# Kernel optimization log

Hardware: AMD Instinct MI355X
Metric: run time of the kernel (lower is better)

The kernel has to match this reference:

```python
import jax, jax.numpy as jnp
import numpy as np

B, S, D, V, ND = 8, 512, 1024, 32000, 8


def setup_inputs() -> dict:
    key = jax.random.key(0)
    k1, k2, k3, k4 = jax.random.split(key, 4)
    scale = 0.02
    return {
        "hidden_states": jax.random.normal(k1, (B, S, D), dtype=jnp.float32),
        "domain_ids": jax.random.randint(k2, (B,), 0, ND + 1),  # index ND triggers default head
        "W_base": jax.random.normal(k3, (D, D), dtype=jnp.float32) * scale,
        "b_base": jnp.zeros((D,), dtype=jnp.float32),
        # slots 0..ND-1 are domain heads, slot ND is the default head
        "W_heads": jax.random.normal(k4, (ND + 1, D, V), dtype=jnp.float32) * scale,
        "b_heads": jnp.zeros((ND + 1, V), dtype=jnp.float32),
    }


def reference(hidden_states, domain_ids, W_base, b_base, W_heads, b_heads):
    # base_projection: Linear(D, D)
    hidden = jnp.einsum("bsd,de->bse", hidden_states, W_base) + b_base
    num_domains = W_heads.shape[0] - 1
    # out-of-range domain ids fall back to the default head (last slot)
    idx = jnp.where((domain_ids >= 0) & (domain_ids < num_domains), domain_ids, num_domains)
    Wg = W_heads[idx]              # [B, D, V] gathered per-example head weights
    bg = b_heads[idx]              # [B, V]
    out = jnp.einsum("bsd,bdv->bsv", hidden, Wg) + bg[:, None, :]
    return out
```

## Files before the change

kernel.cpp:

```cpp
#include <hip/hip_runtime.h>
#include <hip/hip_bf16.h>


#define BCNT 8
#define SLEN 512
#define DDIM 1024
#define VDIM 32000
#define NDOM 8

typedef __attribute__((ext_vector_type(4))) float f32x4;
typedef __attribute__((ext_vector_type(8))) short bf16x8;

static __device__ __forceinline__ unsigned short f2bf(float f) {
    union { float f; unsigned int u; } x; x.f = f;
    unsigned int u = x.u;
    return (unsigned short)((u + 0x7FFFu + ((u >> 16) & 1u)) >> 16);
}

static __device__ __forceinline__ unsigned int pack2(float lo, float hi) {
    float2 t; t.x = lo; t.y = hi;
    union { __hip_bfloat162 h; unsigned int u; } c;
    c.h = __float22bfloat162_rn(t);
    return c.u;
}

#define SBAR()   __builtin_amdgcn_s_barrier()
#define SCHED0() __builtin_amdgcn_sched_barrier(0)

__global__ __launch_bounds__(256)
void gemm1_k(const float* __restrict__ Af, const float* __restrict__ Bbase,
             const float* __restrict__ bias, __hip_bfloat16* __restrict__ Cb,
             int Mrows)
{
    __shared__ __align__(16) __hip_bfloat16 lds_a[128 * 64];
    __shared__ __align__(16) unsigned int   lds_b[32 * 128];

    const int tid  = threadIdx.x;
    const int lane = tid & 63;
    const int w    = tid >> 6;

    const int nwg = gridDim.x;
    const int bid = blockIdx.x;
    const int q   = nwg >> 3;
    const int sid = (bid & 7) * q + (bid >> 3);

    const int MT = Mrows >> 7;
    const int mt = sid % MT;
    const int nt = sid / MT;
    const int m0 = mt << 7;
    const int n0 = nt << 7;

    f32x4 acc[4][4];
    #pragma unroll
    for (int m = 0; m < 4; ++m)
        #pragma unroll
        for (int n = 0; n < 4; ++n)
            acc[m][n] = (f32x4)0.0f;

    const int wr = w >> 1, wc = w & 1;
    const int lr = lane & 15, lg = lane >> 4;

    for (int kt = 0; kt < DDIM / 64; ++kt) {
        const int kbase = kt * 64;

        #pragma unroll
        for (int t = 0; t < 8; ++t) {
            const int flat = (t * 256 + tid) * 4;
            const int row = flat >> 6, col = flat & 63;
            const float4 v = *(const float4*)(Af + (size_t)(m0 + row) * DDIM + kbase + col);
            uint2 pp;
            pp.x = pack2(v.x, v.y);
            pp.y = pack2(v.z, v.w);
            *(uint2*)(lds_a + flat) = pp;
        }

        #pragma unroll
        for (int t = 0; t < 4; ++t) {
            const int id = t * 256 + tid;
            const int kk = id >> 5;
            const int n  = (id & 31) << 2;
            const float* b0 = Bbase + (size_t)(kbase + 2 * kk) * DDIM + n0 + n;
            const float4 e = *(const float4*)b0;
            const float4 o = *(const float4*)(b0 + DDIM);
            uint4 pw;
            pw.x = pack2(e.x, o.x);
            pw.y = pack2(e.y, o.y);
            pw.z = pack2(e.z, o.z);
            pw.w = pack2(e.w, o.w);
            const int ns = n ^ ((kk & 4) << 2);
            *(uint4*)&lds_b[kk * 128 + ns] = pw;
        }

        __syncthreads();

        #pragma unroll
        for (int ks = 0; ks < 2; ++ks) {
            bf16x8 af[4], bfr[4];
            #pragma unroll
            for (int m = 0; m < 4; ++m) {
                const int row = wr * 64 + m * 16 + lr;
                const int k   = ks * 32 + lg * 8;
                af[m] = *(const bf16x8*)&lds_a[row * 64 + k];
            }
            #pragma unroll
            for (int n = 0; n < 4; ++n) {
                const int col = wc * 64 + n * 16 + lr;
                const int kkb = ks * 16 + lg * 4;
                union { unsigned int u[4]; bf16x8 v; } cvt;
                #pragma unroll
                for (int j = 0; j < 4; ++j) {
                    const int kk = kkb + j;
                    const int ns = col ^ ((kk & 4) << 2);
                    cvt.u[j] = lds_b[kk * 128 + ns];
                }
                bfr[n] = cvt.v;
            }
            #pragma unroll
            for (int m = 0; m < 4; ++m)
                #pragma unroll
                for (int n = 0; n < 4; ++n)
                    acc[m][n] = __builtin_amdgcn_mfma_f32_16x16x32_bf16(af[m], bfr[n], acc[m][n], 0, 0, 0);
        }

        __syncthreads();
    }

    #pragma unroll
    for (int m = 0; m < 4; ++m) {
        #pragma unroll
        for (int n = 0; n < 4; ++n) {
            const int col = n0 + wc * 64 + n * 16 + lr;
            const float bv = bias[col];
            #pragma unroll
            for (int r = 0; r < 4; ++r) {
                const int row = m0 + wr * 64 + m * 16 + lg * 4 + r;
                Cb[(size_t)row * DDIM + col] = __hip_bfloat16_raw{f2bf(acc[m][n][r] + bv)};
            }
        }
    }
}

__global__ __launch_bounds__(512, 4)
void gemm2_k(const __hip_bfloat16* __restrict__ A, const float* __restrict__ Wh,
             const float* __restrict__ bh, float* __restrict__ out,
             const int* __restrict__ dom)
{
    __shared__ __align__(16) __hip_bfloat16 ldsA[256 * 64];
    __shared__ __align__(16) unsigned int   ldsB[128 * 32];

    const int tid  = threadIdx.x;
    const int lane = tid & 63;
    const int w    = tid >> 6;
    const int wr   = w >> 1;
    const int wc   = w & 1;
    const int lr   = lane & 15;
    const int lg   = lane >> 4;

    const int bid  = blockIdx.x;
    const int q    = gridDim.x >> 3;
    const int sid  = (bid & 7) * q + (bid >> 3);
    const int mt   = sid & 1;
    const int rest = sid >> 1;
    const int nt   = rest % 250;
    const int ex   = rest / 250;
    const int m0   = ex * SLEN + mt * 256;
    const int n0   = nt * 128;

    const int di  = dom[ex];
    const int hid = (di >= 0 && di < NDOM) ? di : NDOM;
    const float* Bp   = Wh + (size_t)hid * DDIM * (size_t)VDIM;
    const float* bias = bh + (size_t)hid * (size_t)VDIM;

    f32x4 acc[4][4];
    #pragma unroll
    for (int m = 0; m < 4; ++m)
        #pragma unroll
        for (int n = 0; n < 4; ++n)
            acc[m][n] = (f32x4)0.0f;

    const int nb  = (tid & 63) << 1;
    const int kb  = (tid >> 6) << 3;
    const int qb  = kb >> 1;
    const int bsw = (lane & 7) << 2;
    const int bslot = qb ^ bsw;

    float2 br[8];

    #define LOADB(KT) do {                                                         \
        const float* _p = Bp + (size_t)((KT) * 64 + kb) * VDIM + n0 + nb;          \
        _Pragma("unroll")                                                          \
        for (int j = 0; j < 8; ++j) br[j] = *(const float2*)(_p + (size_t)j * VDIM); \
    } while (0)

    #define WRITEB() do {                                                          \
        uint4 w0, w1;                                                              \
        w0.x = pack2(br[0].x, br[1].x); w0.y = pack2(br[2].x, br[3].x);            \
        w0.z = pack2(br[4].x, br[5].x); w0.w = pack2(br[6].x, br[7].x);            \
        w1.x = pack2(br[0].y, br[1].y); w1.y = pack2(br[2].y, br[3].y);            \
        w1.z = pack2(br[4].y, br[5].y); w1.w = pack2(br[6].y, br[7].y);            \
        *(uint4*)&ldsB[nb * 32 + bslot]       = w0;                                \
        *(uint4*)&ldsB[(nb + 1) * 32 + bslot] = w1;                                \
    } while (0)

    #define STAGEA(KT) do {                                                        \
        _Pragma("unroll")                                                          \
        for (int i = 0; i < 4; ++i) {                                              \
            const int base_e = (i * 8 + w) * 512;                                  \
            const int flat   = base_e + lane * 8;                                  \
            const int row    = flat >> 6;                                          \
            const int kbyte  = (flat & 63) * 2;                                    \
            const int srck   = (kbyte ^ ((row & 7) << 4)) >> 1;                    \
            const __hip_bfloat16* src = A + (size_t)(m0 + row) * DDIM + (KT) * 64 + srck; \
            __builtin_amdgcn_global_load_lds(                                      \
                (const __attribute__((address_space(1))) unsigned int*)src,        \
                (__attribute__((address_space(3))) unsigned int*)(ldsA + base_e),  \
                16, 0, 0);                                                         \
        }                                                                          \
    } while (0)

    #define COMPUTE() do {                                                         \
        _Pragma("unroll")                                                          \
        for (int ks = 0; ks < 2; ++ks) {                                           \
            bf16x8 af[4], bfr[4];                                                  \
            _Pragma("unroll")                                                      \
            for (int m = 0; m < 4; ++m) {                                          \
                const int row = wr * 64 + m * 16 + lr;                             \
                const int kby = ks * 64 + lg * 16;                                 \
                const int eff = kby ^ ((row & 7) << 4);                            \
                af[m] = *(const bf16x8*)&ldsA[row * 64 + (eff >> 1)];              \
            }                                                                      \
            _Pragma("unroll")                                                      \
            for (int n = 0; n < 4; ++n) {                                          \
                const int col  = wc * 64 + n * 16 + lr;                            \
                const int kkb  = ks * 16 + lg * 4;                                 \
                const int slot = kkb ^ (((col >> 1) & 7) << 2);                    \
                bfr[n] = *(const bf16x8*)&ldsB[col * 32 + slot];                   \
            }                                                                      \
            _Pragma("unroll")                                                      \
            for (int m = 0; m < 4; ++m)                                            \
                _Pragma("unroll")                                                  \
                for (int n = 0; n < 4; ++n)                                        \
                    acc[m][n] = __builtin_amdgcn_mfma_f32_16x16x32_bf16(af[m], bfr[n], acc[m][n], 0, 0, 0); \
        }                                                                          \
    } while (0)

    LOADB(0);
    SCHED0();
    STAGEA(0);
    SCHED0();
    WRITEB();
    SCHED0();
    LOADB(1);
    SCHED0();
    asm volatile("s_waitcnt vmcnt(8) lgkmcnt(0)" ::: "memory");
    SCHED0();
    SBAR();

    for (int kt = 0; kt < 16; ++kt) {
        COMPUTE();
        if (kt < 15) {
            SCHED0();
            SBAR();
            SCHED0();
            STAGEA(kt + 1);
            SCHED0();
            WRITEB();
            SCHED0();
            if (kt < 14) {
                LOADB(kt + 2);
                SCHED0();
                asm volatile("s_waitcnt vmcnt(8) lgkmcnt(0)" ::: "memory");
            } else {
                asm volatile("s_waitcnt vmcnt(0) lgkmcnt(0)" ::: "memory");
            }
            SCHED0();
            SBAR();
        }
    }

    #pragma unroll
    for (int n = 0; n < 4; ++n) {
        const int col = n0 + wc * 64 + n * 16 + lr;
        const float bv = bias[col];
        #pragma unroll
        for (int m = 0; m < 4; ++m) {
            #pragma unroll
            for (int r = 0; r < 4; ++r) {
                const int row = m0 + wr * 64 + m * 16 + lg * 4 + r;
                out[(size_t)row * VDIM + col] = acc[m][n][r] + bv;
            }
        }
    }

    #undef LOADB
    #undef WRITEB
    #undef STAGEA
    #undef COMPUTE
}

extern "C" void kernel_launch(void* const* d_in, const int* in_sizes, int n_in,
                              void* d_out, int out_size, void* d_ws, size_t ws_size,
                              hipStream_t stream)
{
    const float* hs  = (const float*)d_in[0];
    const int*   dom = (const int*)d_in[1];
    const float* Wb  = (const float*)d_in[2];
    const float* bb  = (const float*)d_in[3];
    const float* Wh  = (const float*)d_in[4];
    const float* bh  = (const float*)d_in[5];
    float* out = (float*)d_out;
    __hip_bfloat16* hidden = (__hip_bfloat16*)d_ws;

    const int M = BCNT * SLEN;

    const int g1 = (M / 128) * (DDIM / 128);
    hipLaunchKernelGGL(gemm1_k, dim3(g1), dim3(256), 0, stream, hs, Wb, bb, hidden, M);

    const int g2 = BCNT * (SLEN / 256) * (VDIM / 128);
    hipLaunchKernelGGL(gemm2_k, dim3(g2), dim3(512), 0, stream, hidden, Wh, bh, out, dom);
}
```

Before: 531.4 us.

## Double-buffer LDS in head GEMM and interleave staging with MFMA half-steps

Switches the second GEMM from single-buffered to double-buffered LDS for both the A and B tiles, using 96KB of dynamic shared memory. Each k-step is split into two halves so global-to-LDS staging for the next tile overlaps with MFMA on the current one, and MFMA phases get raised wave priority. This is meant to hide load and barrier latency, at the cost of halving the occupancy target (launch bounds 4→2) and adding more barriers per iteration.

```diff
diff --git a/kernel.cpp b/kernel.cpp
--- a/kernel.cpp
+++ b/kernel.cpp
@@ -140,13 +140,16 @@
     }
 }
 
-__global__ __launch_bounds__(512, 4)
+__global__ __launch_bounds__(512, 2)
 void gemm2_k(const __hip_bfloat16* __restrict__ A, const float* __restrict__ Wh,
              const float* __restrict__ bh, float* __restrict__ out,
              const int* __restrict__ dom)
 {
-    __shared__ __align__(16) __hip_bfloat16 ldsA[256 * 64];
-    __shared__ __align__(16) unsigned int   ldsB[128 * 32];
+    extern __shared__ __align__(16) char smem[];
+    __hip_bfloat16* ldsA0 = (__hip_bfloat16*)smem;
+    __hip_bfloat16* ldsA1 = (__hip_bfloat16*)(smem + 32768);
+    unsigned int*   ldsB0 = (unsigned int*)(smem + 65536);
+    unsigned int*   ldsB1 = (unsigned int*)(smem + 81920);
 
     const int tid  = threadIdx.x;
     const int lane = tid & 63;
@@ -192,19 +195,19 @@
         for (int j = 0; j < 8; ++j) br[j] = *(const float2*)(_p + (size_t)j * VDIM); \
     } while (0)
 
-    #define WRITEB() do {                                                          \
+    #define WRITEB(LB) do {                                                        \
         uint4 w0, w1;                                                              \
         w0.x = pack2(br[0].x, br[1].x); w0.y = pack2(br[2].x, br[3].x);            \
         w0.z = pack2(br[4].x, br[5].x); w0.w = pack2(br[6].x, br[7].x);            \
         w1.x = pack2(br[0].y, br[1].y); w1.y = pack2(br[2].y, br[3].y);            \
         w1.z = pack2(br[4].y, br[5].y); w1.w = pack2(br[6].y, br[7].y);            \
-        *(uint4*)&ldsB[nb * 32 + bslot]       = w0;                                \
-        *(uint4*)&ldsB[(nb + 1) * 32 + bslot] = w1;                                \
-    } while (0)
-
-    #define STAGEA(KT) do {                                                        \
-        _Pragma("unroll")                                                          \
-        for (int i = 0; i < 4; ++i) {                                              \
+        *(uint4*)&(LB)[nb * 32 + bslot]       = w0;                                \
+        *(uint4*)&(LB)[(nb + 1) * 32 + bslot] = w1;                                \
+    } while (0)
+
+    #define STAGEA_H(LA, KT, H) do {                                               \
+        _Pragma("unroll")                                                          \
+        for (int i = 2*(H); i < 2*(H) + 2; ++i) {                                  \
             const int base_e = (i * 8 + w) * 512;                                  \
             const int flat   = base_e + lane * 8;                                  \
             const int row    = flat >> 6;                                          \
@@ -213,42 +216,42 @@
             const __hip_bfloat16* src = A + (size_t)(m0 + row) * DDIM + (KT) * 64 + srck; \
             __builtin_amdgcn_global_load_lds(                                      \
                 (const __attribute__((address_space(1))) unsigned int*)src,        \
-                (__attribute__((address_space(3))) unsigned int*)(ldsA + base_e),  \
+                (__attribute__((address_space(3))) unsigned int*)((LA) + base_e),  \
                 16, 0, 0);                                                         \
         }                                                                          \
     } while (0)
 
-    #define COMPUTE() do {                                                         \
-        _Pragma("unroll")                                                          \
-        for (int ks = 0; ks < 2; ++ks) {                                           \
-            bf16x8 af[4], bfr[4];                                                  \
+    #define READ_FRAGS(AF, BF, LA, LB, KS) do {                                    \
+        _Pragma("unroll")                                                          \
+        for (int m = 0; m < 4; ++m) {                                              \
+            const int row = wr * 64 + m * 16 + lr;                                 \
+            const int kby = (KS) * 64 + lg * 16;                                   \
+            const int eff = kby ^ ((row & 7) << 4);                                \
+            AF[m] = *(const bf16x8*)&(LA)[row * 64 + (eff >> 1)];                  \
+        }                                                                          \
+        _Pragma("unroll")                                                          \
+        for (int n = 0; n < 4; ++n) {                                              \
+            const int col  = wc * 64 + n * 16 + lr;                                \
+            const int kkb  = (KS) * 16 + lg * 4;                                   \
+            const int slot = kkb ^ (((col >> 1) & 7) << 2);                        \
+            BF[n] = *(const bf16x8*)&(LB)[col * 32 + slot];                        \
+        }                                                                          \
+    } while (0)
+
+    #define MFMA16(AF, BF) do {                                                    \
+        _Pragma("unroll")                                                          \
+        for (int m = 0; m < 4; ++m)                                                \
             _Pragma("unroll")                                                      \
-            for (int m = 0; m < 4; ++m) {                                          \
-                const int row = wr * 64 + m * 16 + lr;                             \
-                const int kby = ks * 64 + lg * 16;                                 \
-                const int eff = kby ^ ((row & 7) << 4);                            \
-                af[m] = *(const bf16x8*)&ldsA[row * 64 + (eff >> 1)];              \
-            }                                                                      \
-            _Pragma("unroll")                                                      \
-            for (int n = 0; n < 4; ++n) {                                          \
-                const int col  = wc * 64 + n * 16 + lr;                            \
-                const int kkb  = ks * 16 + lg * 4;                                 \
-                const int slot = kkb ^ (((col >> 1) & 7) << 2);                    \
-                bfr[n] = *(const bf16x8*)&ldsB[col * 32 + slot];                   \
-            }                                                                      \
-            _Pragma("unroll")                                                      \
-            for (int m = 0; m < 4; ++m)                                            \
-                _Pragma("unroll")                                                  \
-                for (int n = 0; n < 4; ++n)                                        \
-                    acc[m][n] = __builtin_amdgcn_mfma_f32_16x16x32_bf16(af[m], bfr[n], acc[m][n], 0, 0, 0); \
-        }                                                                          \
+            for (int n = 0; n < 4; ++n)                                            \
+                acc[m][n] = __builtin_amdgcn_mfma_f32_16x16x32_bf16(AF[m], BF[n], acc[m][n], 0, 0, 0); \
     } while (0)
 
     LOADB(0);
     SCHED0();
-    STAGEA(0);
-    SCHED0();
-    WRITEB();
+    STAGEA_H(ldsA0, 0, 0);
+    STAGEA_H(ldsA0, 0, 1);
+    SCHED0();
+    WRITEB(ldsB0);
     SCHED0();
     LOADB(1);
     SCHED0();
@@ -257,24 +260,51 @@
     SBAR();
 
     for (int kt = 0; kt < 16; ++kt) {
-        COMPUTE();
-        if (kt < 15) {
-            SCHED0();
+        __hip_bfloat16* lA  = (kt & 1) ? ldsA1 : ldsA0;
+        __hip_bfloat16* lAn = (kt & 1) ? ldsA0 : ldsA1;
+        unsigned int*   lB  = (kt & 1) ? ldsB1 : ldsB0;
+        unsigned int*   lBn = (kt & 1) ? ldsB0 : ldsB1;
+
+        {
+            bf16x8 af[4], bfr[4];
+            READ_FRAGS(af, bfr, lA, lB, 0);
+            SCHED0();
+            if (kt < 15) { STAGEA_H(lAn, kt + 1, 0); SCHED0(); }
             SBAR();
-            SCHED0();
-            STAGEA(kt + 1);
-            SCHED0();
-            WRITEB();
+            asm volatile("s_waitcnt lgkmcnt(0)" ::: "memory");
+            SCHED0();
+            __builtin_amdgcn_s_setprio(1);
+            MFMA16(af, bfr);
+            __builtin_amdgcn_s_setprio(0);
+            SCHED0();
+            SBAR();
+        }
+
+        {
+            bf16x8 af[4], bfr[4];
+            READ_FRAGS(af, bfr, lA, lB, 1);
+            SCHED0();
+            if (kt < 15) {
+                STAGEA_H(lAn, kt + 1, 1);
+                SCHED0();
+                WRITEB(lBn);
+                SCHED0();
+            }
+            if (kt < 14) { LOADB(kt + 2); SCHED0(); }
+            SBAR();
+            asm volatile("s_waitcnt lgkmcnt(0)" ::: "memory");
+            SCHED0();
+            __builtin_amdgcn_s_setprio(1);
+            MFMA16(af, bfr);
+            __builtin_amdgcn_s_setprio(0);
             SCHED0();
             if (kt < 14) {
-                LOADB(kt + 2);
-                SCHED0();
-                asm volatile("s_waitcnt vmcnt(8) lgkmcnt(0)" ::: "memory");
-            } else {
-                asm volatile("s_waitcnt vmcnt(0) lgkmcnt(0)" ::: "memory");
-            }
-            SCHED0();
-            SBAR();
+                asm volatile("s_waitcnt vmcnt(8)" ::: "memory");
+            } else if (kt == 14) {
+                asm volatile("s_waitcnt vmcnt(0)" ::: "memory");
+            }
+            SCHED0();
+            if (kt < 15) SBAR();
         }
     }
 
@@ -294,8 +324,9 @@
 
     #undef LOADB
     #undef WRITEB
-    #undef STAGEA
-    #undef COMPUTE
+    #undef STAGEA_H
+    #undef READ_FRAGS
+    #undef MFMA16
 }
 
 extern "C" void kernel_launch(void* const* d_in, const int* in_sizes, int n_in,
@@ -316,6 +347,12 @@
     const int g1 = (M / 128) * (DDIM / 128);
     hipLaunchKernelGGL(gemm1_k, dim3(g1), dim3(256), 0, stream, hs, Wb, bb, hidden, M);
 
+    const int smem_bytes = 98304;
+    static int attr_set = 0;
+    if (!attr_set) {
+        hipFuncSetAttribute((const void*)gemm2_k, hipFuncAttributeMaxDynamicSharedMemorySize, smem_bytes);
+        attr_set = 1;
+    }
     const int g2 = BCNT * (SLEN / 256) * (VDIM / 128);
-    hipLaunchKernelGGL(gemm2_k, dim3(g2), dim3(512), 0, stream, hidden, Wh, bh, out, dom);
-}
+    hipLaunchKernelGGL(gemm2_k, dim3(g2), dim3(512), smem_bytes, stream, hidden, Wh, bh, out, dom);
+}
```

Result: slower. 578.8 us (+8.9%).
